# Performance work log

Measured on AMD Instinct MI355X. Metric: run time of the kernel, lower is better.

The kernel has to match this reference:

```python
import jax, jax.numpy as jnp
import numpy as np

D = 2048   # embed_dim
E = 128    # expand_ratio = head dim
H = D // E # num heads = 16
C = 64     # chunk size for the chunked linear-attention scan
EPS = 1e-6


def setup_inputs() -> dict:
    key = jax.random.key(0)
    ks = jax.random.split(key, 6)
    b, n = 2, 2048
    s = 0.02
    x = jax.random.normal(ks[0], (b, n, D), jnp.float32)
    Wq = (jax.random.normal(ks[1], (D, D), jnp.float32) * s)
    Wk = (jax.random.normal(ks[2], (D, D), jnp.float32) * s)
    Wv = (jax.random.normal(ks[3], (D, D), jnp.float32) * s)
    Wf = (jax.random.normal(ks[4], (D, H), jnp.float32) * s)
    Wo = (jax.random.normal(ks[5], (D, D), jnp.float32) * s)
    norm_w = jnp.ones((D,), jnp.float32)
    return {"x": x, "Wq": Wq, "Wk": Wk, "Wv": Wv, "Wf": Wf, "Wo": Wo, "norm_w": norm_w}


def _lightning_scalar_decay(q, k, v, ld):
    # q,k,v: [b,n,H,E], ld: [b,n,H] log decay per head per step.
    # Recurrence: S_t = exp(ld_t) * S_{t-1} + k_t^T v_t ; o_t = q_t @ S_t
    b, n, h, e = q.shape
    nc = n // C
    qc = q.reshape(b, nc, C, h, e)
    kc = k.reshape(b, nc, C, h, e)
    vc = v.reshape(b, nc, C, h, e)
    ldc = ld.reshape(b, nc, C, h)
    cum = jnp.cumsum(ldc, axis=2)          # inclusive within-chunk log decay [b,nc,C,h]
    tot = cum[:, :, -1, :]                 # [b,nc,h]

    # intra-chunk: scores[i,j] = (q_i . k_j) * exp(L_i - L_j), j <= i
    Lh = cum.transpose(0, 1, 3, 2)         # [b,nc,h,C]
    decay = jnp.exp(Lh[..., :, None] - Lh[..., None, :])  # [b,nc,h,C,C]
    mask = jnp.tril(jnp.ones((C, C), bool))
    scores = jnp.einsum('bmihe,bmjhe->bmhij', qc, kc) * decay
    scores = jnp.where(mask, scores, 0.0)
    o_intra = jnp.einsum('bmhij,bmjhe->bmihe', scores, vc)

    # inter-chunk: carried recurrent state S [b,h,e,e]
    def step(S, inp):
        q_c, k_c, v_c, cum_c, tot_c = inp  # [b,C,h,e],...,[b,C,h],[b,h]
        o = jnp.einsum('bihe,bhef->bihf', q_c * jnp.exp(cum_c)[..., None], S)
        kd = k_c * jnp.exp(tot_c[:, None, :] - cum_c)[..., None]
        S_new = S * jnp.exp(tot_c)[:, :, None, None] + jnp.einsum('bihe,bihf->bhef', kd, v_c)
        return S_new, o

    xs = (qc.transpose(1, 0, 2, 3, 4), kc.transpose(1, 0, 2, 3, 4),
          vc.transpose(1, 0, 2, 3, 4), cum.transpose(1, 0, 2, 3), tot.transpose(1, 0, 2))
    S0 = jnp.zeros((b, h, e, e), q.dtype)
    S_final, o_inter = jax.lax.scan(step, S0, xs)
    o_inter = o_inter.transpose(1, 0, 2, 3, 4)  # [b,nc,C,h,e]
    return (o_intra + o_inter).reshape(b, n, h * e), S_final


def reference(x, Wq, Wk, Wv, Wf, Wo, norm_w):
    b, n, d = x.shape
    q = jax.nn.silu(x @ Wq).reshape(b, n, H, E)
    k = jax.nn.silu(x @ Wk).reshape(b, n, H, E)
    v = (x @ Wv).reshape(b, n, H, E)
    ld = jax.nn.log_sigmoid(x @ Wf)  # [b,n,H]
    o, _ = _lightning_scalar_decay(q, k, v, ld)
    # RMSNorm over full embed dim
    o = o * jax.lax.rsqrt(jnp.mean(o * o, axis=-1, keepdims=True) + EPS) * norm_w
    return o @ Wo
```

## Files before the change

### kernel.cpp

```cpp
#include <hip/hip_runtime.h>
#include <hip/hip_bf16.h>
#include <stdint.h>

#define D_ 2048
#define E_ 128
#define H_ 16
#define NB_ 2
#define NSEQ_ 2048
#define NTOK_ 4096
#define NCH_ 32

typedef short bf16s;
typedef __attribute__((ext_vector_type(8))) short bf16x8;
typedef __attribute__((ext_vector_type(4))) float f32x4;

__device__ __forceinline__ short f2b(float f) {
  __hip_bfloat16 h = __float2bfloat16(f);
  return *reinterpret_cast<short*>(&h);
}
__device__ __forceinline__ float b2f(short s) {
  __hip_bfloat16 h;
  *reinterpret_cast<short*>(&h) = s;
  return __bfloat162float(h);
}

__device__ __forceinline__ void gload_lds16(const void* g, void* l) {
  __builtin_amdgcn_global_load_lds(
      (__attribute__((address_space(1))) void*)(const_cast<void*>(g)),
      (__attribute__((address_space(3))) void*)(l), 16, 0, 0);
}

template <int N>
__device__ __forceinline__ void wait_vmcnt() {
  if constexpr (N == 0)      asm volatile("s_waitcnt vmcnt(0)" ::: "memory");
  else if constexpr (N == 4) asm volatile("s_waitcnt vmcnt(4)" ::: "memory");
  else static_assert(N == 0, "unsupported vmcnt");
}
__device__ __forceinline__ void lgkm0_fence() {
  asm volatile("s_waitcnt lgkmcnt(0)" ::: "memory");
  __builtin_amdgcn_sched_barrier(0);
}

__global__ __launch_bounds__(256)
void cvt_bf16(const float* __restrict__ x, bf16s* __restrict__ y) {
  const size_t i = (size_t)blockIdx.x * 256 + threadIdx.x;
  const float4 a = ((const float4*)x)[i * 2];
  const float4 b = ((const float4*)x)[i * 2 + 1];
  bf16x8 o;
  o[0] = f2b(a.x); o[1] = f2b(a.y); o[2] = f2b(a.z); o[3] = f2b(a.w);
  o[4] = f2b(b.x); o[5] = f2b(b.y); o[6] = f2b(b.z); o[7] = f2b(b.w);
  *(bf16x8*)&y[i * 8] = o;
}

__global__ __launch_bounds__(256)
void transpose_w(const float* __restrict__ Wq, const float* __restrict__ Wk,
                 const float* __restrict__ Wv, const float* __restrict__ Wo,
                 const float* __restrict__ nw, bf16s* __restrict__ WqT,
                 bf16s* __restrict__ WkT, bf16s* __restrict__ WvT,
                 bf16s* __restrict__ WoT) {
  const float* src; bf16s* dst;
  if (blockIdx.z == 0)      { src = Wq; dst = WqT; }
  else if (blockIdx.z == 1) { src = Wk; dst = WkT; }
  else if (blockIdx.z == 2) { src = Wv; dst = WvT; }
  else                      { src = Wo; dst = WoT; }
  __shared__ float tile[64][65];
  const int n0 = blockIdx.x * 64, k0 = blockIdx.y * 64;
  const int t = threadIdx.x;
  const int tr = t >> 6, tc = t & 63;
#pragma unroll
  for (int rr = 0; rr < 16; ++rr) {
    const int row = rr * 4 + tr;
    tile[row][tc] = src[(size_t)(k0 + row) * D_ + n0 + tc];
  }
  __syncthreads();
  const float wk = (blockIdx.z == 3) ? nw[k0 + tc] : 1.f;
#pragma unroll
  for (int rr = 0; rr < 16; ++rr) {
    const int row = rr * 4 + tr;
    dst[(size_t)(n0 + row) * D_ + k0 + tc] = f2b(tile[tc][row] * wk);
  }
}

__global__ __launch_bounds__(256)
void ld_gemm(const float* __restrict__ x, const float* __restrict__ Wf,
             float* __restrict__ ldb) {
  const int t = threadIdx.x;
  const int col = t & 15;
  const int tok = blockIdx.x * 16 + (t >> 4);
  const float4* xr = (const float4*)(x + (size_t)tok * D_);
  float s = 0.f;
#pragma unroll 4
  for (int kk = 0; kk < D_ / 4; ++kk) {
    const float4 xv = xr[kk];
    const int k4 = kk * 4;
    s += xv.x * Wf[(k4 + 0) * H_ + col];
    s += xv.y * Wf[(k4 + 1) * H_ + col];
    s += xv.z * Wf[(k4 + 2) * H_ + col];
    s += xv.w * Wf[(k4 + 3) * H_ + col];
  }
  const float m = fminf(s, 0.f);
  ldb[(size_t)tok * H_ + col] = m - log1pf(__expf(-fabsf(s)));
}

__global__ __launch_bounds__(512, 2)
void gemm_qkv8p(const bf16s* __restrict__ xb, const bf16s* __restrict__ WqT,
                const bf16s* __restrict__ WkT, const bf16s* __restrict__ WvT,
                bf16s* __restrict__ qb, bf16s* __restrict__ kb,
                bf16s* __restrict__ vb) {
  const int bn = blockIdx.x, bm = blockIdx.y, z = blockIdx.z;
  const bf16s* Bt; bf16s* outp; int act;
  if (z == 0)      { Bt = WqT; outp = qb; act = 1; }
  else if (z == 1) { Bt = WkT; outp = kb; act = 1; }
  else             { Bt = WvT; outp = vb; act = 0; }

  __shared__ bf16s As[2 * 256 * 64];
  __shared__ bf16s Bs[2 * 256 * 64];
  const int t = threadIdx.x;
  const int w = t >> 6, l = t & 63;
  const int wm = w >> 2, wn = w & 3;
  const int lr = l & 15, lk = l >> 4;

  const size_t abase = (size_t)(bm * 256) * D_;
  const size_t bbase = (size_t)(bn * 256) * D_;

  f32x4 acc[8][4] = {};

  auto stageHT = [&](int m, int part) {
    const int slot = m & 1;
    const int k0 = m * 64;
    const int rowoff = (part >> 1) * 128;
    const bool isB = part & 1;
    const bf16s* g = isB ? Bt : xb;
    const size_t gb = (isB ? bbase : abase) + (size_t)rowoff * D_ + k0;
    bf16s* lb = (isB ? Bs : As) + slot * (256 * 64) + rowoff * 64;
#pragma unroll
    for (int rr = 0; rr < 2; ++rr) {
      const int r = rr * 64 + (t >> 3);
      const int cs = (t & 7) ^ (r & 7);
      gload_lds16(&g[gb + (size_t)r * D_ + cs * 8], &lb[rr * 4096 + w * 512]);
    }
  };
  auto ldA = [&](int slot, int fm, int ks) -> bf16x8 {
    const int row = fm * 32 + wm * 16 + lr;
    return *(const bf16x8*)&As[slot * (256 * 64) + row * 64 +
                               (((ks << 2) + lk) ^ (row & 7)) * 8];
  };
  auto ldB = [&](int slot, int fn, int ks) -> bf16x8 {
    const int row = fn * 64 + wn * 16 + lr;
    return *(const bf16x8*)&Bs[slot * (256 * 64) + row * 64 +
                               (((ks << 2) + lk) ^ (row & 7)) * 8];
  };

  stageHT(0, 0); stageHT(0, 1); stageHT(0, 2); stageHT(0, 3);
  stageHT(1, 0); stageHT(1, 1);
  wait_vmcnt<4>();
  __builtin_amdgcn_s_barrier();

  bf16x8 af[4][2], bf0[2][2], bf1[2][2];
  for (int j = 0; j < 32; ++j) {
    const int s = j & 1;
#pragma unroll
    for (int fm = 0; fm < 4; ++fm)
#pragma unroll
      for (int ks = 0; ks < 2; ++ks) af[fm][ks] = ldA(s, fm, ks);
#pragma unroll
    for (int fn = 0; fn < 2; ++fn)
#pragma unroll
      for (int ks = 0; ks < 2; ++ks) {
        bf0[fn][ks] = ldB(s, fn, ks);
        bf1[fn][ks] = ldB(s, fn + 2, ks);
      }
    if (j <= 30) { stageHT(j + 1, 3); stageHT(j + 1, 2); }
    __builtin_amdgcn_s_barrier();
    lgkm0_fence();
    __builtin_amdgcn_s_setprio(1);
#pragma unroll
    for (int fm = 0; fm < 4; ++fm)
#pragma unroll
      for (int fn = 0; fn < 2; ++fn)
#pragma unroll
        for (int ks = 0; ks < 2; ++ks) {
          acc[fm][fn] = __builtin_amdgcn_mfma_f32_16x16x32_bf16(
              af[fm][ks], bf0[fn][ks], acc[fm][fn], 0, 0, 0);
          acc[fm][fn + 2] = __builtin_amdgcn_mfma_f32_16x16x32_bf16(
              af[fm][ks], bf1[fn][ks], acc[fm][fn + 2], 0, 0, 0);
        }
    __builtin_amdgcn_s_setprio(0);
    __builtin_amdgcn_s_barrier();
#pragma unroll
    for (int fm = 0; fm < 4; ++fm)
#pragma unroll
      for (int ks = 0; ks < 2; ++ks) af[fm][ks] = ldA(s, fm + 4, ks);
    if (j <= 29) { stageHT(j + 2, 0); stageHT(j + 2, 1); }
    __builtin_amdgcn_s_barrier();
    lgkm0_fence();
    __builtin_amdgcn_s_setprio(1);
#pragma unroll
    for (int fm = 0; fm < 4; ++fm)
#pragma unroll
      for (int fn = 0; fn < 2; ++fn)
#pragma unroll
        for (int ks = 0; ks < 2; ++ks) {
          acc[fm + 4][fn + 2] = __builtin_amdgcn_mfma_f32_16x16x32_bf16(
              af[fm][ks], bf1[fn][ks], acc[fm + 4][fn + 2], 0, 0, 0);
          acc[fm + 4][fn] = __builtin_amdgcn_mfma_f32_16x16x32_bf16(
              af[fm][ks], bf0[fn][ks], acc[fm + 4][fn], 0, 0, 0);
        }
    __builtin_amdgcn_s_setprio(0);
    if (j <= 29)      wait_vmcnt<4>();
    else if (j == 30) wait_vmcnt<0>();
    __builtin_amdgcn_s_barrier();
  }

#pragma unroll
  for (int fm = 0; fm < 8; ++fm) {
    const int row = bm * 256 + fm * 32 + wm * 16 + lk * 4;
#pragma unroll
    for (int fn = 0; fn < 4; ++fn) {
      const int col = bn * 256 + fn * 64 + wn * 16 + lr;
#pragma unroll
      for (int r = 0; r < 4; ++r) {
        float vv = acc[fm][fn][r];
        if (act) vv = vv / (1.f + __expf(-vv));
        outp[(size_t)(row + r) * D_ + col] = f2b(vv);
      }
    }
  }
}

__device__ __forceinline__ void gemm_body128(const bf16s* __restrict__ A,
                                             const bf16s* __restrict__ Bt,
                                             float* __restrict__ Cm, int bm,
                                             int bn, const float* __restrict__ rs) {
  constexpr int BK = 64;
  __shared__ bf16s As[128 * BK];
  __shared__ bf16s Bs[128 * BK];
  const int t = threadIdx.x;
  const int w = t >> 6, l = t & 63;
  const int wm = w >> 1, wn = w & 1;
  const int lr = l & 15, lk = l >> 4;
  const int sr8 = l >> 3, sc = l & 7;
  const int cs = sc ^ sr8;
  f32x4 acc[4][4] = {};

  const size_t abase = (size_t)(bm * 128) * D_;
  const size_t bbase = (size_t)(bn * 128) * D_;

  for (int k0 = 0; k0 < D_; k0 += BK) {
    __syncthreads();
#pragma unroll
    for (int j = 0; j < 4; ++j) {
      const int row = w * 32 + j * 8;
      gload_lds16(&A[abase + (size_t)(row + sr8) * D_ + k0 + cs * 8],
                  &As[row * BK]);
      gload_lds16(&Bt[bbase + (size_t)(row + sr8) * D_ + k0 + cs * 8],
                  &Bs[row * BK]);
    }
    __syncthreads();
    bf16x8 af[4][2], bfr[4][2];
#pragma unroll
    for (int tm = 0; tm < 4; ++tm) {
      const int row = wm * 64 + tm * 16 + lr;
#pragma unroll
      for (int ks = 0; ks < 2; ++ks)
        af[tm][ks] =
            *(const bf16x8*)&As[row * BK + ((ks * 4 + lk) ^ (row & 7)) * 8];
    }
#pragma unroll
    for (int tn = 0; tn < 4; ++tn) {
      const int row = wn * 64 + tn * 16 + lr;
#pragma unroll
      for (int ks = 0; ks < 2; ++ks)
        bfr[tn][ks] =
            *(const bf16x8*)&Bs[row * BK + ((ks * 4 + lk) ^ (row & 7)) * 8];
    }
#pragma unroll
    for (int ks = 0; ks < 2; ++ks)
#pragma unroll
      for (int tm = 0; tm < 4; ++tm)
#pragma unroll
        for (int tn = 0; tn < 4; ++tn)
          acc[tm][tn] = __builtin_amdgcn_mfma_f32_16x16x32_bf16(
              af[tm][ks], bfr[tn][ks], acc[tm][tn], 0, 0, 0);
  }

#pragma unroll
  for (int tm = 0; tm < 4; ++tm) {
    const int rowb = bm * 128 + wm * 64 + tm * 16 + lk * 4;
#pragma unroll
    for (int tn = 0; tn < 4; ++tn) {
      const int col = bn * 128 + wn * 64 + tn * 16 + lr;
#pragma unroll
      for (int r = 0; r < 4; ++r) {
        float vv = acc[tm][tn][r] * rs[rowb + r];
        Cm[(size_t)(rowb + r) * D_ + col] = vv;
      }
    }
  }
}

__global__ __launch_bounds__(256)
void gemm_out(const bf16s* __restrict__ A, const bf16s* __restrict__ Bt,
              const float* __restrict__ rs, float* __restrict__ out) {
  const int orig = blockIdx.x;
  const int lin = (orig & 7) * 64 + (orig >> 3);
  const int bm = lin & 31;
  const int bn = lin >> 5;
  gemm_body128(A, Bt, out, bm, bn, rs);
}

__global__ __launch_bounds__(256)
void chunk_state(const bf16s* __restrict__ k, const bf16s* __restrict__ v,
                 const float* __restrict__ ldp, bf16s* __restrict__ Mbuf,
                 float* __restrict__ totb) {
  const int c = blockIdx.x, bh = blockIdx.y;
  const int b = bh >> 4, h = bh & 15;
  const int t = threadIdx.x;
  const int w = t >> 6, l = t & 63;
  const int lr = l & 15, lk = l >> 4;

  __shared__ bf16s Kt[64 * 128];
  __shared__ bf16s Vn[64 * 128];
  __shared__ bf16s KdT[128 * 64];
  __shared__ bf16s VtT[128 * 64];
  __shared__ float cumS[64];
  char* cKt = (char*)Kt; char* cVn = (char*)Vn;
  char* cKdT = (char*)KdT; char* cVtT = (char*)VtT;

  const size_t grow0 = (size_t)b * NSEQ_ + c * 64;
#pragma unroll
  for (int j = 0; j < 4; ++j) {
    const int lrow = w * 16 + j * 4 + (l >> 4);
    const int ck = (l & 15) ^ (lrow & 7);
    const size_t goff = (grow0 + lrow) * D_ + h * E_ + ck * 8;
    const int lbase = (w * 16 + j * 4) * 128;
    gload_lds16(&k[goff], &Kt[lbase]);
    gload_lds16(&v[goff], &Vn[lbase]);
  }
  if (w == 0) {
    float val = ldp[(grow0 + l) * H_ + h];
#pragma unroll
    for (int off = 1; off < 64; off <<= 1) {
      float pv = __shfl_up(val, off);
      if (l >= off) val += pv;
    }
    cumS[l] = val;
  }
  __syncthreads();
  const float tot = cumS[63];
  if (t == 0) totb[bh * NCH_ + c] = tot;

#pragma unroll
  for (int it = 0; it < 4; ++it) {
    const int task = t + it * 256;
    const int i = task >> 4, cx = task & 15;
    const int sb = i * 256 + ((cx * 16) ^ ((i & 7) << 4));
    bf16x8 vv = *(const bf16x8*)(cVn + sb);
    bf16x8 kk8 = *(const bf16x8*)(cKt + sb);
    const float sE = __expf(tot - cumS[i]);
#pragma unroll
    for (int jj = 0; jj < 8; ++jj) {
      const int e = cx * 8 + jj;
      const int db = e * 128 + ((i * 2) ^ ((e & 7) << 4));
      *(bf16s*)(cVtT + db) = vv[jj];
      *(bf16s*)(cKdT + db) = f2b(b2f(kk8[jj]) * sE);
    }
  }
  __syncthreads();

  const int wm = w >> 1, wn = w & 1;
  f32x4 acc[4][4] = {};
#pragma unroll
  for (int kk2 = 0; kk2 < 2; ++kk2) {
    const int cb = (kk2 * 32 + lk * 8) * 2;
    bf16x8 af[4], bfr[4];
#pragma unroll
    for (int tm = 0; tm < 4; ++tm) {
      const int fr = wm * 64 + tm * 16 + lr;
      af[tm] = *(const bf16x8*)(cVtT + fr * 128 + (cb ^ ((fr & 7) << 4)));
    }
#pragma unroll
    for (int tn = 0; tn < 4; ++tn) {
      const int er = wn * 64 + tn * 16 + lr;
      bfr[tn] = *(const bf16x8*)(cKdT + er * 128 + (cb ^ ((er & 7) << 4)));
    }
#pragma unroll
    for (int tm = 0; tm < 4; ++tm)
#pragma unroll
      for (int tn = 0; tn < 4; ++tn)
        acc[tm][tn] = __builtin_amdgcn_mfma_f32_16x16x32_bf16(
            af[tm], bfr[tn], acc[tm][tn], 0, 0, 0);
  }
  const size_t mb = (size_t)(bh * NCH_ + c) * 128 * 128;
#pragma unroll
  for (int tm = 0; tm < 4; ++tm) {
#pragma unroll
    for (int tn = 0; tn < 4; ++tn) {
#pragma unroll
      for (int r = 0; r < 4; ++r) {
        const int f = wm * 64 + tm * 16 + lk * 4 + r;
        const int e = wn * 64 + tn * 16 + lr;
        Mbuf[mb + f * 128 + e] = f2b(acc[tm][tn][r]);
      }
    }
  }
}

__global__ __launch_bounds__(256)
void state_scan(const bf16s* __restrict__ Mbuf, const float* __restrict__ totb,
                bf16s* __restrict__ Sbuf) {
  const int sl = blockIdx.x;
  const int bh = blockIdx.y;
  const int t = threadIdx.x;
  const int fr = sl * 16 + (t >> 4);
  const int e0 = (t & 15) * 8;
  const size_t base = ((size_t)(bh * NCH_) * 128 + fr) * 128 + e0;
  const size_t cstride = 128 * 128;
  __shared__ float tots[NCH_];
  if (t < NCH_) tots[t] = totb[bh * NCH_ + t];
  __syncthreads();
  float acc[8] = {};
  bf16x8 m0 = *(const bf16x8*)&Mbuf[base + 0 * cstride];
  bf16x8 m1 = *(const bf16x8*)&Mbuf[base + 1 * cstride];
  bf16x8 m2 = *(const bf16x8*)&Mbuf[base + 2 * cstride];
  bf16x8 m3 = *(const bf16x8*)&Mbuf[base + 3 * cstride];
#pragma unroll
  for (int c = 0; c < NCH_; ++c) {
    bf16x8 sv;
#pragma unroll
    for (int j = 0; j < 8; ++j) sv[j] = f2b(acc[j]);
    *(bf16x8*)&Sbuf[base + (size_t)c * cstride] = sv;
    const bf16x8 mc = ((c & 3) == 0) ? m0 : ((c & 3) == 1) ? m1
                     : ((c & 3) == 2) ? m2 : m3;
    const float dt = __expf(tots[c]);
#pragma unroll
    for (int j = 0; j < 8; ++j) acc[j] = acc[j] * dt + b2f(mc[j]);
    if (c + 4 < NCH_) {
      const bf16x8 mn = *(const bf16x8*)&Mbuf[base + (size_t)(c + 4) * cstride];
      if ((c & 3) == 0) m0 = mn;
      else if ((c & 3) == 1) m1 = mn;
      else if ((c & 3) == 2) m2 = mn;
      else m3 = mn;
    }
  }
}

__global__ __launch_bounds__(256)
void attn_out(const bf16s* __restrict__ q, const bf16s* __restrict__ k,
              const bf16s* __restrict__ v, const float* __restrict__ ldp,
              const bf16s* __restrict__ Sbuf, bf16s* __restrict__ o) {
  const int c = blockIdx.x, bh = blockIdx.y;
  const int b = bh >> 4, h = bh & 15;
  const int t = threadIdx.x;
  const int w = t >> 6, l = t & 63;
  const int lr = l & 15, lk = l >> 4;

  __shared__ bf16s Qt[64 * 128];
  __shared__ bf16s Kt[64 * 128];
  __shared__ bf16s Vn[64 * 128];
  __shared__ bf16s VtT[128 * 64];
  __shared__ bf16s Pm[64 * 64];
  __shared__ float cumS[64];
  char* cQt = (char*)Qt; char* cKt = (char*)Kt; char* cVn = (char*)Vn;
  char* cVtT = (char*)VtT; char* cPm = (char*)Pm;

  const size_t grow0 = (size_t)b * NSEQ_ + c * 64;
  const size_t sbase = (size_t)(bh * NCH_ + c) * 128 * 128;
  const bf16x8* Sp = (const bf16x8*)&Sbuf[sbase];
#pragma unroll
  for (int j = 0; j < 4; ++j) {
    const int lrow = w * 16 + j * 4 + (l >> 4);
    const int ck = (l & 15) ^ (lrow & 7);
    const size_t goff = (grow0 + lrow) * D_ + h * E_ + ck * 8;
    const int lbase = (w * 16 + j * 4) * 128;
    gload_lds16(&q[goff], &Qt[lbase]);
    gload_lds16(&k[goff], &Kt[lbase]);
    gload_lds16(&v[goff], &Vn[lbase]);
  }
  if (w == 0) {
    float val = ldp[(grow0 + l) * H_ + h];
#pragma unroll
    for (int off = 1; off < 64; off <<= 1) {
      float pv = __shfl_up(val, off);
      if (l >= off) val += pv;
    }
    cumS[l] = val;
  }
  __syncthreads();

#pragma unroll
  for (int it = 0; it < 4; ++it) {
    const int task = t + it * 256;
    const int i = task >> 4, cx = task & 15;
    const int sb = i * 256 + ((cx * 16) ^ ((i & 7) << 4));
    bf16x8 vv = *(const bf16x8*)(cVn + sb);
#pragma unroll
    for (int jj = 0; jj < 8; ++jj) {
      const int e = cx * 8 + jj;
      const int db = e * 128 + ((i * 2) ^ ((e & 7) << 4));
      *(bf16s*)(cVtT + db) = vv[jj];
    }
  }

  f32x4 accs[4] = {};
  f32x4 acco[8] = {};
#pragma unroll
  for (int kk = 0; kk < 4; ++kk) {
    const int cb = (kk * 32 + lk * 8) * 2;
    const int ar = w * 16 + lr;
    bf16x8 aq = *(const bf16x8*)(cQt + ar * 256 + (cb ^ ((ar & 7) << 4)));
#pragma unroll
    for (int tn = 0; tn < 4; ++tn) {
      const int br = tn * 16 + lr;
      bf16x8 bk = *(const bf16x8*)(cKt + br * 256 + (cb ^ ((br & 7) << 4)));
      accs[tn] = __builtin_amdgcn_mfma_f32_16x16x32_bf16(aq, bk, accs[tn], 0, 0, 0);
    }
#pragma unroll
    for (int tf = 0; tf < 8; ++tf) {
      bf16x8 bs = Sp[(tf * 16 + lr) * 16 + kk * 4 + lk];
      acco[tf] = __builtin_amdgcn_mfma_f32_16x16x32_bf16(aq, bs, acco[tf], 0, 0, 0);
    }
  }
#pragma unroll
  for (int r = 0; r < 4; ++r) {
    const float gI = __expf(cumS[w * 16 + lk * 4 + r]);
#pragma unroll
    for (int tf = 0; tf < 8; ++tf) acco[tf][r] *= gI;
  }
#pragma unroll
  for (int tn = 0; tn < 4; ++tn) {
    const int j = tn * 16 + lr;
    const float cj = cumS[j];
#pragma unroll
    for (int r = 0; r < 4; ++r) {
      const int i = w * 16 + lk * 4 + r;
      const float sv = (j <= i) ? accs[tn][r] * __expf(cumS[i] - cj) : 0.f;
      *(bf16s*)(cPm + i * 128 + ((j * 2) ^ ((i & 7) << 4))) = f2b(sv);
    }
  }
  __syncthreads();

#pragma unroll
  for (int kk2 = 0; kk2 < 2; ++kk2) {
    const int cb = (kk2 * 32 + lk * 8) * 2;
    const int pr = w * 16 + lr;
    bf16x8 ap = *(const bf16x8*)(cPm + pr * 128 + (cb ^ ((pr & 7) << 4)));
#pragma unroll
    for (int tf = 0; tf < 8; ++tf) {
      const int fr = tf * 16 + lr;
      bf16x8 bv = *(const bf16x8*)(cVtT + fr * 128 + (cb ^ ((fr & 7) << 4)));
      acco[tf] = __builtin_amdgcn_mfma_f32_16x16x32_bf16(ap, bv, acco[tf], 0, 0, 0);
    }
  }
#pragma unroll
  for (int tf = 0; tf < 8; ++tf) {
#pragma unroll
    for (int r = 0; r < 4; ++r) {
      const int i = w * 16 + lk * 4 + r;
      o[(grow0 + i) * D_ + h * E_ + tf * 16 + lr] = f2b(acco[tf][r]);
    }
  }
}

__global__ __launch_bounds__(256)
void rms_scale(const bf16s* __restrict__ o, float* __restrict__ sout) {
  const int tok = blockIdx.x;
  const int t = threadIdx.x;
  bf16x8 vv = *(const bf16x8*)&o[(size_t)tok * D_ + t * 8];
  float s = 0.f;
#pragma unroll
  for (int j = 0; j < 8; ++j) { const float f = b2f(vv[j]); s += f * f; }
#pragma unroll
  for (int off2 = 32; off2 > 0; off2 >>= 1) s += __shfl_down(s, off2);
  __shared__ float wsum[4];
  if ((t & 63) == 0) wsum[t >> 6] = s;
  __syncthreads();
  if (t == 0)
    sout[tok] = rsqrtf((wsum[0] + wsum[1] + wsum[2] + wsum[3]) * (1.f / D_) +
                       1e-6f);
}

extern "C" void kernel_launch(void* const* d_in, const int* in_sizes, int n_in,
                              void* d_out, int out_size, void* d_ws,
                              size_t ws_size, hipStream_t stream) {
  (void)in_sizes; (void)n_in; (void)out_size;
  const float* x  = (const float*)d_in[0];
  const float* Wq = (const float*)d_in[1];
  const float* Wk = (const float*)d_in[2];
  const float* Wv = (const float*)d_in[3];
  const float* Wf = (const float*)d_in[4];
  const float* Wo = (const float*)d_in[5];
  const float* nw = (const float*)d_in[6];
  float* out = (float*)d_out;

  char* ws = (char*)d_ws;
  const size_t MB = 1024 * 1024;
  bf16s* xb   = (bf16s*)(ws + 0);
  bf16s* WqT  = (bf16s*)(ws + 16 * MB);
  bf16s* WkT  = (bf16s*)(ws + 24 * MB);
  bf16s* WvT  = (bf16s*)(ws + 32 * MB);
  bf16s* Sbuf = (bf16s*)(ws + 0);
  float* totb = (float*)(ws + 32 * MB);
  bf16s* WoT  = (bf16s*)(ws + 40 * MB);
  bf16s* qb   = (bf16s*)(ws + 48 * MB);
  bf16s* kb   = (bf16s*)(ws + 64 * MB);
  bf16s* vb   = (bf16s*)(ws + 80 * MB);
  bf16s* ob   = (bf16s*)(ws + 96 * MB);
  bf16s* Mbuf = (bf16s*)(ws + 112 * MB);
  float* ldb  = (float*)(ws + 144 * MB);
  float* rsb  = (float*)(ws + 145 * MB);
  if (146 * MB > ws_size) return;

  cvt_bf16<<<NTOK_ * D_ / 8 / 256, 256, 0, stream>>>(x, xb);
  transpose_w<<<dim3(32, 32, 4), 256, 0, stream>>>(Wq, Wk, Wv, Wo, nw, WqT,
                                                   WkT, WvT, WoT);
  ld_gemm<<<NTOK_ / 16, 256, 0, stream>>>(x, Wf, ldb);
  gemm_qkv8p<<<dim3(8, 16, 3), 512, 0, stream>>>(xb, WqT, WkT, WvT, qb, kb, vb);
  chunk_state<<<dim3(NCH_, NB_ * H_), 256, 0, stream>>>(kb, vb, ldb, Mbuf, totb);
  state_scan<<<dim3(8, NB_ * H_), 256, 0, stream>>>(Mbuf, totb, Sbuf);
  attn_out<<<dim3(NCH_, NB_ * H_), 256, 0, stream>>>(qb, kb, vb, ldb, Sbuf, ob);
  rms_scale<<<NTOK_, 256, 0, stream>>>(ob, rsb);
  gemm_out<<<512, 256, 0, stream>>>(ob, WoT, rsb, out);
}
```

Measured before the change: 298.8 us.

## Fuse Q/K/V projections into one GEMM sharing A tiles, triple-buffered BK=32

```diff
diff --git a/kernel.cpp b/kernel.cpp
--- a/kernel.cpp
+++ b/kernel.cpp
@@ -32,8 +32,9 @@
 
 template <int N>
 __device__ __forceinline__ void wait_vmcnt() {
-  if constexpr (N == 0)      asm volatile("s_waitcnt vmcnt(0)" ::: "memory");
-  else if constexpr (N == 4) asm volatile("s_waitcnt vmcnt(4)" ::: "memory");
+  if constexpr (N == 0)       asm volatile("s_waitcnt vmcnt(0)" ::: "memory");
+  else if constexpr (N == 5)  asm volatile("s_waitcnt vmcnt(5)" ::: "memory");
+  else if constexpr (N == 10) asm volatile("s_waitcnt vmcnt(10)" ::: "memory");
   else static_assert(N == 0, "unsupported vmcnt");
 }
 __device__ __forceinline__ void lgkm0_fence() {
@@ -103,126 +104,118 @@
 }
 
 __global__ __launch_bounds__(512, 2)
-void gemm_qkv8p(const bf16s* __restrict__ xb, const bf16s* __restrict__ WqT,
-                const bf16s* __restrict__ WkT, const bf16s* __restrict__ WvT,
-                bf16s* __restrict__ qb, bf16s* __restrict__ kb,
-                bf16s* __restrict__ vb) {
-  const int bn = blockIdx.x, bm = blockIdx.y, z = blockIdx.z;
-  const bf16s* Bt; bf16s* outp; int act;
-  if (z == 0)      { Bt = WqT; outp = qb; act = 1; }
-  else if (z == 1) { Bt = WkT; outp = kb; act = 1; }
-  else             { Bt = WvT; outp = vb; act = 0; }
-
-  __shared__ bf16s As[2 * 256 * 64];
-  __shared__ bf16s Bs[2 * 256 * 64];
+void gemm_qkv_fz(const bf16s* __restrict__ xb, const bf16s* __restrict__ WqT,
+                 const bf16s* __restrict__ WkT, const bf16s* __restrict__ WvT,
+                 bf16s* __restrict__ qb, bf16s* __restrict__ kb,
+                 bf16s* __restrict__ vb) {
+  const int bn = blockIdx.x & 15, bm = blockIdx.x >> 4;
+  __shared__ bf16s As[3 * 256 * 32];
+  __shared__ bf16s Bs[3 * 3 * 128 * 32];
   const int t = threadIdx.x;
   const int w = t >> 6, l = t & 63;
-  const int wm = w >> 2, wn = w & 3;
+  const int wm = w >> 1, wn = w & 1;
   const int lr = l & 15, lk = l >> 4;
+  const int srow = t >> 2;
+  const int scs = (t & 3) ^ ((srow >> 1) & 3);
 
   const size_t abase = (size_t)(bm * 256) * D_;
-  const size_t bbase = (size_t)(bn * 256) * D_;
-
-  f32x4 acc[8][4] = {};
-
-  auto stageHT = [&](int m, int part) {
-    const int slot = m & 1;
-    const int k0 = m * 64;
-    const int rowoff = (part >> 1) * 128;
-    const bool isB = part & 1;
-    const bf16s* g = isB ? Bt : xb;
-    const size_t gb = (isB ? bbase : abase) + (size_t)rowoff * D_ + k0;
-    bf16s* lb = (isB ? Bs : As) + slot * (256 * 64) + rowoff * 64;
-#pragma unroll
-    for (int rr = 0; rr < 2; ++rr) {
-      const int r = rr * 64 + (t >> 3);
-      const int cs = (t & 7) ^ (r & 7);
-      gload_lds16(&g[gb + (size_t)r * D_ + cs * 8], &lb[rr * 4096 + w * 512]);
-    }
+  const size_t bbase = (size_t)(bn * 128) * D_;
+
+  f32x4 acc[3][4][4] = {};
+
+  auto stageA = [&](int m, int slot, int p) {
+    const int k0 = m * 32;
+    gload_lds16(&xb[abase + (size_t)(p * 128 + srow) * D_ + k0 + scs * 8],
+                &As[slot * 8192 + p * 4096 + w * 512]);
   };
-  auto ldA = [&](int slot, int fm, int ks) -> bf16x8 {
-    const int row = fm * 32 + wm * 16 + lr;
-    return *(const bf16x8*)&As[slot * (256 * 64) + row * 64 +
-                               (((ks << 2) + lk) ^ (row & 7)) * 8];
+  auto stageB = [&](int m, int slot, int z, const bf16s* Wt) {
+    const int k0 = m * 32;
+    gload_lds16(&Wt[bbase + (size_t)srow * D_ + k0 + scs * 8],
+                &Bs[slot * 12288 + z * 4096 + w * 512]);
   };
-  auto ldB = [&](int slot, int fn, int ks) -> bf16x8 {
-    const int row = fn * 64 + wn * 16 + lr;
-    return *(const bf16x8*)&Bs[slot * (256 * 64) + row * 64 +
-                               (((ks << 2) + lk) ^ (row & 7)) * 8];
+  auto ldA = [&](int slot, int fm) -> bf16x8 {
+    const int row = wm * 64 + fm * 16 + lr;
+    return *(const bf16x8*)&As[slot * 8192 + row * 32 +
+                               (lk ^ ((row >> 1) & 3)) * 8];
   };
-
-  stageHT(0, 0); stageHT(0, 1); stageHT(0, 2); stageHT(0, 3);
-  stageHT(1, 0); stageHT(1, 1);
-  wait_vmcnt<4>();
+  auto ldB = [&](int slot, int z, int fn) -> bf16x8 {
+    const int row = wn * 64 + fn * 16 + lr;
+    return *(const bf16x8*)&Bs[slot * 12288 + z * 4096 + row * 32 +
+                               (lk ^ ((row >> 1) & 3)) * 8];
+  };
+
+#pragma unroll
+  for (int m = 0; m < 3; ++m) {
+    stageA(m, m, 0); stageA(m, m, 1);
+    stageB(m, m, 0, WqT); stageB(m, m, 1, WkT); stageB(m, m, 2, WvT);
+  }
+  wait_vmcnt<10>();
   __builtin_amdgcn_s_barrier();
 
-  bf16x8 af[4][2], bf0[2][2], bf1[2][2];
-  for (int j = 0; j < 32; ++j) {
-    const int s = j & 1;
-#pragma unroll
-    for (int fm = 0; fm < 4; ++fm)
-#pragma unroll
-      for (int ks = 0; ks < 2; ++ks) af[fm][ks] = ldA(s, fm, ks);
-#pragma unroll
-    for (int fn = 0; fn < 2; ++fn)
-#pragma unroll
-      for (int ks = 0; ks < 2; ++ks) {
-        bf0[fn][ks] = ldB(s, fn, ks);
-        bf1[fn][ks] = ldB(s, fn + 2, ks);
-      }
-    if (j <= 30) { stageHT(j + 1, 3); stageHT(j + 1, 2); }
-    __builtin_amdgcn_s_barrier();
+  int slot = 0, slot2 = 2;
+  for (int j = 0; j < 64; ++j) {
+    bf16x8 af[4], bfr[4];
+#pragma unroll
+    for (int fm = 0; fm < 4; ++fm) af[fm] = ldA(slot, fm);
+#pragma unroll
+    for (int fn = 0; fn < 4; ++fn) bfr[fn] = ldB(slot, 0, fn);
+    if (j <= 61) { stageA(j + 2, slot2, 0); stageA(j + 2, slot2, 1);
+                   stageB(j + 2, slot2, 0, WqT); }
     lgkm0_fence();
     __builtin_amdgcn_s_setprio(1);
 #pragma unroll
     for (int fm = 0; fm < 4; ++fm)
 #pragma unroll
-      for (int fn = 0; fn < 2; ++fn)
-#pragma unroll
-        for (int ks = 0; ks < 2; ++ks) {
-          acc[fm][fn] = __builtin_amdgcn_mfma_f32_16x16x32_bf16(
-              af[fm][ks], bf0[fn][ks], acc[fm][fn], 0, 0, 0);
-          acc[fm][fn + 2] = __builtin_amdgcn_mfma_f32_16x16x32_bf16(
-              af[fm][ks], bf1[fn][ks], acc[fm][fn + 2], 0, 0, 0);
-        }
+      for (int fn = 0; fn < 4; ++fn)
+        acc[0][fm][fn] = __builtin_amdgcn_mfma_f32_16x16x32_bf16(
+            af[fm], bfr[fn], acc[0][fm][fn], 0, 0, 0);
     __builtin_amdgcn_s_setprio(0);
-    __builtin_amdgcn_s_barrier();
-#pragma unroll
-    for (int fm = 0; fm < 4; ++fm)
-#pragma unroll
-      for (int ks = 0; ks < 2; ++ks) af[fm][ks] = ldA(s, fm + 4, ks);
-    if (j <= 29) { stageHT(j + 2, 0); stageHT(j + 2, 1); }
-    __builtin_amdgcn_s_barrier();
+#pragma unroll
+    for (int fn = 0; fn < 4; ++fn) bfr[fn] = ldB(slot, 1, fn);
+    if (j <= 61) stageB(j + 2, slot2, 1, WkT);
     lgkm0_fence();
     __builtin_amdgcn_s_setprio(1);
 #pragma unroll
     for (int fm = 0; fm < 4; ++fm)
 #pragma unroll
-      for (int fn = 0; fn < 2; ++fn)
-#pragma unroll
-        for (int ks = 0; ks < 2; ++ks) {
-          acc[fm + 4][fn + 2] = __builtin_amdgcn_mfma_f32_16x16x32_bf16(
-              af[fm][ks], bf1[fn][ks], acc[fm + 4][fn + 2], 0, 0, 0);
-          acc[fm + 4][fn] = __builtin_amdgcn_mfma_f32_16x16x32_bf16(
-              af[fm][ks], bf0[fn][ks], acc[fm + 4][fn], 0, 0, 0);
+      for (int fn = 0; fn < 4; ++fn)
+        acc[1][fm][fn] = __builtin_amdgcn_mfma_f32_16x16x32_bf16(
+            af[fm], bfr[fn], acc[1][fm][fn], 0, 0, 0);
+    __builtin_amdgcn_s_setprio(0);
+#pragma unroll
+    for (int fn = 0; fn < 4; ++fn) bfr[fn] = ldB(slot, 2, fn);
+    if (j <= 61) stageB(j + 2, slot2, 2, WvT);
+    lgkm0_fence();
+    __builtin_amdgcn_s_setprio(1);
+#pragma unroll
+    for (int fm = 0; fm < 4; ++fm)
+#pragma unroll
+      for (int fn = 0; fn < 4; ++fn)
+        acc[2][fm][fn] = __builtin_amdgcn_mfma_f32_16x16x32_bf16(
+            af[fm], bfr[fn], acc[2][fm][fn], 0, 0, 0);
+    __builtin_amdgcn_s_setprio(0);
+    if (j <= 61)      wait_vmcnt<5>();
+    else if (j == 62) wait_vmcnt<0>();
+    __builtin_amdgcn_s_barrier();
+    slot = (slot == 2) ? 0 : slot + 1;
+    slot2 = (slot2 == 2) ? 0 : slot2 + 1;
+  }
+
+#pragma unroll
+  for (int z = 0; z < 3; ++z) {
+    bf16s* outp = (z == 0) ? qb : (z == 1) ? kb : vb;
+#pragma unroll
+    for (int fm = 0; fm < 4; ++fm) {
+      const int row = bm * 256 + wm * 64 + fm * 16 + lk * 4;
+#pragma unroll
+      for (int fn = 0; fn < 4; ++fn) {
+        const int col = bn * 128 + wn * 64 + fn * 16 + lr;
+#pragma unroll
+        for (int r = 0; r < 4; ++r) {
+          float vv = acc[z][fm][fn][r];
+          if (z < 2) vv = vv / (1.f + __expf(-vv));
+          outp[(size_t)(row + r) * D_ + col] = f2b(vv);
         }
-    __builtin_amdgcn_s_setprio(0);
-    if (j <= 29)      wait_vmcnt<4>();
-    else if (j == 30) wait_vmcnt<0>();
-    __builtin_amdgcn_s_barrier();
-  }
-
-#pragma unroll
-  for (int fm = 0; fm < 8; ++fm) {
-    const int row = bm * 256 + fm * 32 + wm * 16 + lk * 4;
-#pragma unroll
-    for (int fn = 0; fn < 4; ++fn) {
-      const int col = bn * 256 + fn * 64 + wn * 16 + lr;
-#pragma unroll
-      for (int r = 0; r < 4; ++r) {
-        float vv = acc[fm][fn][r];
-        if (act) vv = vv / (1.f + __expf(-vv));
-        outp[(size_t)(row + r) * D_ + col] = f2b(vv);
       }
     }
   }
@@ -615,7 +608,7 @@
   transpose_w<<<dim3(32, 32, 4), 256, 0, stream>>>(Wq, Wk, Wv, Wo, nw, WqT,
                                                    WkT, WvT, WoT);
   ld_gemm<<<NTOK_ / 16, 256, 0, stream>>>(x, Wf, ldb);
-  gemm_qkv8p<<<dim3(8, 16, 3), 512, 0, stream>>>(xb, WqT, WkT, WvT, qb, kb, vb);
+  gemm_qkv_fz<<<256, 512, 0, stream>>>(xb, WqT, WkT, WvT, qb, kb, vb);
   chunk_state<<<dim3(NCH_, NB_ * H_), 256, 0, stream>>>(kb, vb, ldb, Mbuf, totb);
   state_scan<<<dim3(8, NB_ * H_), 256, 0, stream>>>(Mbuf, totb, Sbuf);
   attn_out<<<dim3(NCH_, NB_ * H_), 256, 0, stream>>>(qb, kb, vb, ldb, Sbuf, ob);
```

Result: faster. 275.8 us (-7.7%).
